# Optimization experiments

Hardware: AMD Instinct MI355X
Metric: run time of the kernel (lower is better)

Reference implementation:

```python
import jax, jax.numpy as jnp
import numpy as np

BATCH_SIZE = 512
N_PARTS = 4
TEMP_FAC = 0.1
D = 4096
EPS = 1e-6


def _static_indices():
    # bs and factor per the n_parts==4, batch_size!=12 branch
    bs = 4 * BATCH_SIZE
    factor = 10 * N_PARTS
    pos = np.arange(bs)
    active = pos[pos % (3 * N_PARTS) < N_PARTS]            # positions that contribute
    # i1..i6 = (pos + k*n_parts) % bs for k = 0..5
    I = (active[:, None] + np.arange(6)[None, :] * N_PARTS) % bs   # (P, 6)
    # denominator indices removed: (pos + k*n_parts) % bs for k = 0..factor*n_parts-1
    offs = (active[:, None] + np.arange(factor * N_PARTS)[None, :] * N_PARTS) % bs
    M = np.ones((active.shape[0], bs), dtype=np.float32)
    M[np.arange(active.shape[0])[:, None], offs] = 0.0     # (P, bs) denominator mask
    return I, M

_I, _M = _static_indices()
# symmetrical-loss pairs: (i1,i2),(i2,i3),(i1,i4),(i4,i5),(i5,i6),(i2,i5),(i3,i6)
_PAIRS = [(0, 1), (1, 2), (0, 3), (3, 4), (4, 5), (1, 4), (2, 5)]


def setup_inputs() -> dict:
    key = jax.random.key(0)
    reg_pred = jax.random.normal(key, (4 * BATCH_SIZE, D), dtype=jnp.float32)
    return {"reg_pred": reg_pred}


def reference(reg_pred):
    I = jnp.asarray(_I)
    M = jnp.asarray(_M)
    norms = jnp.linalg.norm(reg_pred, axis=1)              # (bs,)
    # torch CosineSimilarity: dot / max(||a||*||b||, eps)
    gram = reg_pred @ reg_pred.T                           # (bs, bs)
    S = gram / jnp.maximum(norms[:, None] * norms[None, :], EPS) / TEMP_FAC
    E = jnp.exp(S)                                         # (bs, bs)
    # denominator exp-sums for each anchor role k at each active position p
    Dsum = jnp.einsum('pkb,pb->pk', E[I], M)               # (P, 6)
    total = jnp.float32(0.0)
    for a, b in _PAIRS:
        num = S[I[:, a], I[:, b]]                          # (P,)
        en = jnp.exp(num)
        total = total + jnp.sum(-jnp.log(en / (en + Dsum[:, a]))
                                - jnp.log(en / (en + Dsum[:, b])))
    return total / (6 * BATCH_SIZE)
```

## Files before the change

### kernel.cpp

```cpp
#include <hip/hip_runtime.h>
#include <hip/hip_bf16.h>
#include <stdint.h>

#define NROWS 2048
#define DIM   4096
#define NACT  684
#define INV_TEMP 10.0f
#define NTILE 136
#define KSPLIT 4
#define KSEG  1024
#define KIT   16
#define FP8_SCALE 16.0f
#define PART_SCALE (1.0f / 256.0f)

#define WAITCNT_VM0   0x0F70
#define WAITCNT_VM4   0x0F74
#define WAITCNT_VM8   0x0F78

typedef __attribute__((ext_vector_type(4))) float floatx4;
typedef __attribute__((ext_vector_type(16))) float floatx16;
typedef __attribute__((ext_vector_type(4))) int intx4;
typedef __attribute__((ext_vector_type(8))) int intx8;
typedef __attribute__((ext_vector_type(8))) short shortx8;
typedef __attribute__((ext_vector_type(8))) unsigned short ushortx8;

static __device__ __forceinline__ unsigned short f32_to_bf16(float f) {
  union { float f; unsigned int u; } v; v.f = f;
  unsigned int u = v.u;
  unsigned int r = u + 0x7fffu + ((u >> 16) & 1u);
  return (unsigned short)(r >> 16);
}
static __device__ __forceinline__ float bf16_to_f32(unsigned short u) {
  union { unsigned int u; float f; } v; v.u = ((unsigned int)u) << 16;
  return v.f;
}
static __device__ __forceinline__ unsigned short f32_to_f16(float f) {
  _Float16 h = (_Float16)f;
  union { _Float16 h; unsigned short u; } v; v.h = h;
  return v.u;
}
static __device__ __forceinline__ float f16_to_f32(unsigned short u) {
  union { unsigned short u; _Float16 h; } v; v.u = u;
  return (float)v.h;
}

__global__ __launch_bounds__(256) void k_normconv_fp8(const float* __restrict__ X,
                                                      unsigned char* __restrict__ Yq,
                                                      float* __restrict__ T,
                                                      float* __restrict__ out) {
  const int row = blockIdx.x;
  if (threadIdx.x == 0) T[row] = 0.f;
  if (row == 0 && threadIdx.x == 64) *out = 0.f;
  const float4* xr = (const float4*)(X + (size_t)row * DIM);
  float4 v[4];
  float s = 0.f;
#pragma unroll
  for (int t = 0; t < 4; t++) {
    float4 w = xr[threadIdx.x + t * 256];
    v[t] = w;
    s += w.x * w.x + w.y * w.y + w.z * w.z + w.w * w.w;
  }
#pragma unroll
  for (int off = 32; off > 0; off >>= 1) s += __shfl_down(s, off, 64);
  __shared__ float wsum[4];
  if ((threadIdx.x & 63) == 0) wsum[threadIdx.x >> 6] = s;
  __syncthreads();
  const float total = wsum[0] + wsum[1] + wsum[2] + wsum[3];
  const float sc = FP8_SCALE / fmaxf(sqrtf(total), 1e-30f);
  unsigned int* yr = (unsigned int*)(Yq + (size_t)row * DIM);
#pragma unroll
  for (int t = 0; t < 4; t++) {
    float4 w = v[t];
    unsigned int r0 = __builtin_amdgcn_cvt_pk_fp8_f32(w.x * sc, w.y * sc, 0, false);
    r0 = __builtin_amdgcn_cvt_pk_fp8_f32(w.z * sc, w.w * sc, r0, true);
    yr[threadIdx.x + t * 256] = r0;
  }
}

__global__ __launch_bounds__(256) void k_gemm_mx(const unsigned char* __restrict__ Yq,
                                                 unsigned short* __restrict__ P) {
  __shared__ __attribute__((aligned(16))) unsigned char lds[3 * 16384];
  const int bid0 = blockIdx.x;
  const int bid = (bid0 & 7) * 68 + (bid0 >> 3);
  const int kz = bid & 3;
  const int t  = bid >> 2;
  int ti = 0, rem = t;
  while (rem >= 16 - ti) { rem -= 16 - ti; ti++; }
  const int tj = ti + rem;
  const int row0 = ti * 128;
  const int col0 = tj * 128;
  const int kbase = kz * KSEG;

  const int tid  = threadIdx.x;
  const int lane = tid & 63;
  const int wave = tid >> 6;
  const int wr = wave >> 1;
  const int wc = wave & 1;

  floatx16 zero = {0.f, 0.f, 0.f, 0.f, 0.f, 0.f, 0.f, 0.f,
                   0.f, 0.f, 0.f, 0.f, 0.f, 0.f, 0.f, 0.f};
  floatx16 acc[2][2];
#pragma unroll
  for (int i = 0; i < 2; i++)
#pragma unroll
    for (int j = 0; j < 2; j++) acc[i][j] = zero;

  const int r2  = tid >> 2;
  const int c16 = tid & 3;
  const unsigned int swst = (unsigned)(((r2 >> 1) & 3) << 4);
  const unsigned int colst = ((unsigned)(c16 << 4)) ^ swst;
  const unsigned char* gA = Yq + (size_t)(row0 + r2) * DIM + kbase + colst;
  const unsigned char* gB = Yq + (size_t)(col0 + r2) * DIM + kbase + colst;

#define ISSUE(st, koff)                                                                  \
  do {                                                                                   \
    __builtin_amdgcn_global_load_lds(                                                    \
        (const __attribute__((address_space(1))) void*)(gA + (koff)),                    \
        (__attribute__((address_space(3))) void*)(lds + (st) * 16384 + tid * 16),        \
        16, 0, 0);                                                                       \
    __builtin_amdgcn_global_load_lds(                                                    \
        (const __attribute__((address_space(1))) void*)(gA + (size_t)64 * DIM + (koff)), \
        (__attribute__((address_space(3))) void*)(lds + (st) * 16384 + 4096 + tid * 16), \
        16, 0, 0);                                                                       \
    __builtin_amdgcn_global_load_lds(                                                    \
        (const __attribute__((address_space(1))) void*)(gB + (koff)),                    \
        (__attribute__((address_space(3))) void*)(lds + (st) * 16384 + 8192 + tid * 16), \
        16, 0, 0);                                                                       \
    __builtin_amdgcn_global_load_lds(                                                    \
        (const __attribute__((address_space(1))) void*)(gB + (size_t)64 * DIM + (koff)), \
        (__attribute__((address_space(3))) void*)(lds + (st) * 16384 + 12288 + tid * 16),\
        16, 0, 0);                                                                       \
  } while (0)

#define COMPUTE(st)                                                                      \
  do {                                                                                   \
    const unsigned char* bA = lds + (st) * 16384;                                        \
    const unsigned char* bB = bA + 8192;                                                 \
    const unsigned int c0 = (unsigned)((lane >> 5) << 5);                                \
    intx8 af[2], bf[2];                                                                  \
    _Pragma("unroll")                                                                    \
    for (int mi = 0; mi < 2; mi++) {                                                     \
      const int r = wr * 64 + mi * 32 + (lane & 31);                                     \
      const unsigned int sw = (unsigned)(((r >> 1) & 3) << 4);                           \
      const unsigned char* base = bA + r * 64;                                           \
      intx4 lo = *(const intx4*)(base + (c0 ^ sw));                                      \
      intx4 hi = *(const intx4*)(base + ((c0 ^ sw) ^ 16u));                              \
      intx8 v;                                                                           \
      v[0] = lo[0]; v[1] = lo[1]; v[2] = lo[2]; v[3] = lo[3];                            \
      v[4] = hi[0]; v[5] = hi[1]; v[6] = hi[2]; v[7] = hi[3];                            \
      af[mi] = v;                                                                        \
    }                                                                                    \
    _Pragma("unroll")                                                                    \
    for (int ni = 0; ni < 2; ni++) {                                                     \
      const int r = wc * 64 + ni * 32 + (lane & 31);                                     \
      const unsigned int sw = (unsigned)(((r >> 1) & 3) << 4);                           \
      const unsigned char* base = bB + r * 64;                                           \
      intx4 lo = *(const intx4*)(base + (c0 ^ sw));                                      \
      intx4 hi = *(const intx4*)(base + ((c0 ^ sw) ^ 16u));                              \
      intx8 v;                                                                           \
      v[0] = lo[0]; v[1] = lo[1]; v[2] = lo[2]; v[3] = lo[3];                            \
      v[4] = hi[0]; v[5] = hi[1]; v[6] = hi[2]; v[7] = hi[3];                            \
      bf[ni] = v;                                                                        \
    }                                                                                    \
    _Pragma("unroll")                                                                    \
    for (int mi = 0; mi < 2; mi++)                                                       \
      _Pragma("unroll")                                                                  \
      for (int ni = 0; ni < 2; ni++)                                                     \
        acc[mi][ni] = __builtin_amdgcn_mfma_scale_f32_32x32x64_f8f6f4(                   \
            af[mi], bf[ni], acc[mi][ni], 0, 0, 0, 0x7F7F7F7F, 0, 0x7F7F7F7F);            \
  } while (0)

  ISSUE(0, 0);
  ISSUE(1, 64);
#pragma unroll
  for (int k = 0; k < KIT; k++) {
    const int cur = k % 3;
    if (k < KIT - 2) {
      ISSUE((k + 2) % 3, (k + 2) * 64);
      __builtin_amdgcn_s_waitcnt(WAITCNT_VM8);
    } else if (k == KIT - 2) {
      __builtin_amdgcn_s_waitcnt(WAITCNT_VM4);
    } else {
      __builtin_amdgcn_s_waitcnt(WAITCNT_VM0);
    }
    __builtin_amdgcn_sched_barrier(0);
    __builtin_amdgcn_s_barrier();
    COMPUTE(cur);
    if (k < KIT - 1) {
      __builtin_amdgcn_s_barrier();
      __builtin_amdgcn_sched_barrier(0);
    }
  }

#undef ISSUE
#undef COMPUTE

  unsigned short* dst = P + (size_t)(t * KSPLIT + kz) * 16384;
  const int cc = lane & 31;
  const int cr = (lane >> 5) * 4;
#pragma unroll
  for (int mi = 0; mi < 2; mi++) {
#pragma unroll
    for (int ni = 0; ni < 2; ni++) {
      const int col = wc * 64 + ni * 32 + cc;
#pragma unroll
      for (int q = 0; q < 4; q++) {
        const int row = wr * 64 + mi * 32 + q * 8 + cr;
        unsigned int d0 = (unsigned int)f32_to_bf16(acc[mi][ni][q * 4 + 0] * PART_SCALE) |
                          ((unsigned int)f32_to_bf16(acc[mi][ni][q * 4 + 1] * PART_SCALE) << 16);
        unsigned int d1 = (unsigned int)f32_to_bf16(acc[mi][ni][q * 4 + 2] * PART_SCALE) |
                          ((unsigned int)f32_to_bf16(acc[mi][ni][q * 4 + 3] * PART_SCALE) << 16);
        uint2 v; v.x = d0; v.y = d1;
        *(uint2*)(dst + (size_t)col * 128 + row) = v;
      }
    }
  }
}

__global__ __launch_bounds__(256) void k_combine(const unsigned short* __restrict__ P,
                                                 unsigned short* __restrict__ S,
                                                 float* __restrict__ T) {
  __shared__ float tileS[32][132];
  __shared__ float tileE[32][132];
  const int t = blockIdx.x;
  const int h = blockIdx.y;
  int ti = 0, rem = t;
  while (rem >= 16 - ti) { rem -= 16 - ti; ti++; }
  const int tj = ti + rem;
  const int gr = ti * 128, gc = tj * 128;
  const int c0 = h * 32;
  const int tid = threadIdx.x;
  const int cl = tid >> 3;
  const int q  = tid & 7;

  float acc[16];
#pragma unroll
  for (int j = 0; j < 16; j++) acc[j] = 0.f;
#pragma unroll
  for (int kz = 0; kz < KSPLIT; kz++) {
    const ushortx8* p = (const ushortx8*)(P + (size_t)(t * KSPLIT + kz) * 16384 +
                                          (size_t)(c0 + cl) * 128 + q * 16);
#pragma unroll
    for (int c = 0; c < 2; c++) {
      ushortx8 u = p[c];
#pragma unroll
      for (int e = 0; e < 8; e++) acc[c * 8 + e] += bf16_to_f32((unsigned short)u[e]);
    }
  }
  float cs = 0.f;
  unsigned short hv[16];
#pragma unroll
  for (int j = 0; j < 16; j++) {
    float v = acc[j] * INV_TEMP;
    float ev = __expf(v);
    hv[j] = f32_to_f16(v);
    tileS[cl][q * 16 + j] = v;
    tileE[cl][q * 16 + j] = ev;
    cs += ev;
  }
  {
    uint4* srow = (uint4*)(S + (size_t)(gc + c0 + cl) * NROWS + gr + q * 16);
#pragma unroll
    for (int u = 0; u < 2; u++) {
      uint4 w;
      w.x = (unsigned int)hv[u * 8 + 0] | ((unsigned int)hv[u * 8 + 1] << 16);
      w.y = (unsigned int)hv[u * 8 + 2] | ((unsigned int)hv[u * 8 + 3] << 16);
      w.z = (unsigned int)hv[u * 8 + 4] | ((unsigned int)hv[u * 8 + 5] << 16);
      w.w = (unsigned int)hv[u * 8 + 6] | ((unsigned int)hv[u * 8 + 7] << 16);
      srow[u] = w;
    }
  }
  cs += __shfl_xor(cs, 1, 64);
  cs += __shfl_xor(cs, 2, 64);
  cs += __shfl_xor(cs, 4, 64);
  if (q == 0) atomicAdd(&T[gc + c0 + cl], cs);

  if (ti != tj) {
    __syncthreads();
    const int r = tid >> 1;
    const int hh = tid & 1;
    float rs = 0.f;
    unsigned short hv2[16];
#pragma unroll
    for (int e = 0; e < 16; e++) {
      hv2[e] = f32_to_f16(tileS[hh * 16 + e][r]);
      rs += tileE[hh * 16 + e][r];
    }
    uint4* drow = (uint4*)(S + (size_t)(gr + r) * NROWS + gc + c0 + hh * 16);
#pragma unroll
    for (int u = 0; u < 2; u++) {
      uint4 w;
      w.x = (unsigned int)hv2[u * 8 + 0] | ((unsigned int)hv2[u * 8 + 1] << 16);
      w.y = (unsigned int)hv2[u * 8 + 2] | ((unsigned int)hv2[u * 8 + 3] << 16);
      w.z = (unsigned int)hv2[u * 8 + 4] | ((unsigned int)hv2[u * 8 + 5] << 16);
      w.w = (unsigned int)hv2[u * 8 + 6] | ((unsigned int)hv2[u * 8 + 7] << 16);
      drow[u] = w;
    }
    rs += __shfl_xor(rs, 1, 64);
    if (hh == 0) atomicAdd(&T[gr + r], rs);
  }
}

__global__ __launch_bounds__(384) void k_tail(const unsigned short* __restrict__ S,
                                              const float* __restrict__ T,
                                              float* __restrict__ out) {
  __shared__ float ds_s[6];
  const int p = blockIdx.x;
  const int a = 12 * (p >> 2) + (p & 3);
  const int tid = threadIdx.x;
  const int k = tid >> 6;
  const int lane = tid & 63;
  const int row = (a + 4 * k) & (NROWS - 1);
  const int m = a >> 2;
  const int c = a & 3;
  const uint2* sr = (const uint2*)(S + (size_t)row * NROWS);
  float s = 0.f;
  {
    uint2 v0 = sr[(m + lane) & 511];
    uint2 v1 = sr[(m + 64 + lane) & 511];
    unsigned short e0 = (c < 2) ? (unsigned short)(v0.x >> (16 * c))
                                : (unsigned short)(v0.y >> (16 * (c - 2)));
    unsigned short e1 = (c < 2) ? (unsigned short)(v1.x >> (16 * c))
                                : (unsigned short)(v1.y >> (16 * (c - 2)));
    s += __expf(f16_to_f32(e0)) + __expf(f16_to_f32(e1));
    if (lane < 32) {
      uint2 v2 = sr[(m + 128 + lane) & 511];
      unsigned short e2 = (c < 2) ? (unsigned short)(v2.x >> (16 * c))
                                  : (unsigned short)(v2.y >> (16 * (c - 2)));
      s += __expf(f16_to_f32(e2));
    }
  }
#pragma unroll
  for (int off = 32; off > 0; off >>= 1) s += __shfl_down(s, off, 64);
  if (lane == 0) ds_s[k] = T[row] - s;
  __syncthreads();

  float r = 0.f;
  if (tid < 7) {
    const int pa[7] = {0, 1, 0, 3, 4, 1, 2};
    const int pb[7] = {1, 2, 3, 4, 5, 4, 5};
    const int ra = (a + 4 * pa[tid]) & (NROWS - 1);
    const int rb = (a + 4 * pb[tid]) & (NROWS - 1);
    const float num = f16_to_f32(S[(size_t)ra * NROWS + rb]);
    const float en = __expf(num);
    r = __logf(en + ds_s[pa[tid]]) + __logf(en + ds_s[pb[tid]]) - 2.f * num;
  }
  if (tid < 64) {
    r += __shfl_down(r, 4, 64);
    r += __shfl_down(r, 2, 64);
    r += __shfl_down(r, 1, 64);
    if (tid == 0) atomicAdd(out, r * (1.0f / (6.0f * 512.0f)));
  }
}

__global__ __launch_bounds__(256) void k_normconv(const float* __restrict__ X,
                                                  unsigned short* __restrict__ Y) {
  const int row = blockIdx.x;
  const float4* xr = (const float4*)(X + (size_t)row * DIM);
  float4 v[4];
  float s = 0.f;
#pragma unroll
  for (int t = 0; t < 4; t++) {
    float4 w = xr[threadIdx.x + t * 256];
    v[t] = w;
    s += w.x * w.x + w.y * w.y + w.z * w.z + w.w * w.w;
  }
#pragma unroll
  for (int off = 32; off > 0; off >>= 1) s += __shfl_down(s, off, 64);
  __shared__ float wsum[4];
  if ((threadIdx.x & 63) == 0) wsum[threadIdx.x >> 6] = s;
  __syncthreads();
  const float total = wsum[0] + wsum[1] + wsum[2] + wsum[3];
  const float inv = 1.0f / fmaxf(sqrtf(total), 1e-30f);
  ushort4* yr = (ushort4*)(Y + (size_t)row * DIM);
#pragma unroll
  for (int t = 0; t < 4; t++) {
    float4 w = v[t];
    ushort4 o;
    o.x = f32_to_bf16(w.x * inv);
    o.y = f32_to_bf16(w.y * inv);
    o.z = f32_to_bf16(w.z * inv);
    o.w = f32_to_bf16(w.w * inv);
    yr[threadIdx.x + t * 256] = o;
  }
}

__global__ __launch_bounds__(256) void k_gemm(const unsigned short* __restrict__ Y,
                                              float* __restrict__ S) {
  __shared__ __attribute__((aligned(16))) unsigned short sA[128 * 32];
  __shared__ __attribute__((aligned(16))) unsigned short sB[128 * 32];
  const int tid  = threadIdx.x;
  const int lane = tid & 63;
  const int wave = tid >> 6;
  const int wr = wave >> 1;
  const int wc = wave & 1;
  const int row0 = blockIdx.y * 128;
  const int col0 = blockIdx.x * 128;

  floatx4 zero = {0.f, 0.f, 0.f, 0.f};
  floatx4 acc[4][4];
#pragma unroll
  for (int i = 0; i < 4; i++)
#pragma unroll
    for (int j = 0; j < 4; j++) acc[i][j] = zero;

  const int sr = tid >> 2;
  const int sc = (tid & 3) * 8;
  const unsigned short* gA0 = Y + (size_t)(row0 + sr) * DIM + sc;
  const unsigned short* gA1 = gA0 + (size_t)64 * DIM;
  const unsigned short* gB0 = Y + (size_t)(col0 + sr) * DIM + sc;
  const unsigned short* gB1 = gB0 + (size_t)64 * DIM;

  const int fr = lane & 15;
  const int fc = (lane >> 4) * 8;

  for (int k0 = 0; k0 < DIM; k0 += 32) {
    __builtin_amdgcn_global_load_lds(
        (const __attribute__((address_space(1))) void*)(gA0 + k0),
        (__attribute__((address_space(3))) void*)(sA + tid * 8), 16, 0, 0);
    __builtin_amdgcn_global_load_lds(
        (const __attribute__((address_space(1))) void*)(gA1 + k0),
        (__attribute__((address_space(3))) void*)(sA + 2048 + tid * 8), 16, 0, 0);
    __builtin_amdgcn_global_load_lds(
        (const __attribute__((address_space(1))) void*)(gB0 + k0),
        (__attribute__((address_space(3))) void*)(sB + tid * 8), 16, 0, 0);
    __builtin_amdgcn_global_load_lds(
        (const __attribute__((address_space(1))) void*)(gB1 + k0),
        (__attribute__((address_space(3))) void*)(sB + 2048 + tid * 8), 16, 0, 0);
    __syncthreads();

    shortx8 af[4], bf[4];
#pragma unroll
    for (int mi = 0; mi < 4; mi++)
      af[mi] = *(const shortx8*)(sA + (wr * 64 + mi * 16 + fr) * 32 + fc);
#pragma unroll
    for (int ni = 0; ni < 4; ni++)
      bf[ni] = *(const shortx8*)(sB + (wc * 64 + ni * 16 + fr) * 32 + fc);
#pragma unroll
    for (int mi = 0; mi < 4; mi++)
#pragma unroll
      for (int ni = 0; ni < 4; ni++)
        acc[mi][ni] = __builtin_amdgcn_mfma_f32_16x16x32_bf16(af[mi], bf[ni], acc[mi][ni], 0, 0, 0);
    __syncthreads();
  }

  const int cc  = lane & 15;
  const int cr4 = (lane >> 4) * 4;
#pragma unroll
  for (int mi = 0; mi < 4; mi++) {
    const int row = row0 + wr * 64 + mi * 16 + cr4;
#pragma unroll
    for (int ni = 0; ni < 4; ni++) {
      const int col = col0 + wc * 64 + ni * 16 + cc;
      float* dst = S + (size_t)row * NROWS + col;
#pragma unroll
      for (int r = 0; r < 4; r++) dst[(size_t)r * NROWS] = acc[mi][ni][r] * INV_TEMP;
    }
  }
}

__global__ __launch_bounds__(256) void k_rowsum(const float* __restrict__ S,
                                                float* __restrict__ T) {
  const int row = blockIdx.x;
  const float* sr = S + (size_t)row * NROWS;
  float s = 0.f;
  for (int b = threadIdx.x; b < NROWS; b += 256) s += __expf(sr[b]);
#pragma unroll
  for (int off = 32; off > 0; off >>= 1) s += __shfl_down(s, off, 64);
  __shared__ float wsum[4];
  if ((threadIdx.x & 63) == 0) wsum[threadIdx.x >> 6] = s;
  __syncthreads();
  if (threadIdx.x == 0) T[row] = wsum[0] + wsum[1] + wsum[2] + wsum[3];
}

__global__ __launch_bounds__(64) void k_dsum(const float* __restrict__ S,
                                             const float* __restrict__ T,
                                             float* __restrict__ Ds) {
  const int p = blockIdx.x;
  const int k = blockIdx.y;
  const int a = 12 * (p >> 2) + (p & 3);
  const int lane = threadIdx.x;
  const int row = (a + 4 * k) & (NROWS - 1);
  const int m = a >> 2;
  const int c = a & 3;
  const float4* sr4 = (const float4*)(S + (size_t)row * NROWS);
  float s = 0.f;
  {
    float4 v0 = sr4[(m + lane) & 511];
    float4 v1 = sr4[(m + 64 + lane) & 511];
    float e0 = c == 0 ? v0.x : c == 1 ? v0.y : c == 2 ? v0.z : v0.w;
    float e1 = c == 0 ? v1.x : c == 1 ? v1.y : c == 2 ? v1.z : v1.w;
    s += __expf(e0) + __expf(e1);
    if (lane < 32) {
      float4 v2 = sr4[(m + 128 + lane) & 511];
      float e2 = c == 0 ? v2.x : c == 1 ? v2.y : c == 2 ? v2.z : v2.w;
      s += __expf(e2);
    }
  }
#pragma unroll
  for (int off = 32; off > 0; off >>= 1) s += __shfl_down(s, off, 64);
  if (lane == 0) Ds[p * 6 + k] = T[row] - s;
}

__global__ __launch_bounds__(256) void k_final(const float* __restrict__ S,
                                               const float* __restrict__ Ds,
                                               float* __restrict__ out) {
  const int pa[7] = {0, 1, 0, 3, 4, 1, 2};
  const int pb[7] = {1, 2, 3, 4, 5, 4, 5};
  const int idx = blockIdx.x * 256 + threadIdx.x;
  float s = 0.f;
  if (idx < NACT * 7) {
    const int p = idx / 7;
    const int q = idx - p * 7;
    const int a0 = 12 * (p >> 2) + (p & 3);
    const int ra = (a0 + 4 * pa[q]) & (NROWS - 1);
    const int rb = (a0 + 4 * pb[q]) & (NROWS - 1);
    const float num = S[(size_t)ra * NROWS + rb];
    const float en = __expf(num);
    s = __logf(en + Ds[p * 6 + pa[q]]) + __logf(en + Ds[p * 6 + pb[q]]) - 2.f * num;
  }
#pragma unroll
  for (int off = 32; off > 0; off >>= 1) s += __shfl_down(s, off, 64);
  if ((threadIdx.x & 63) == 0) atomicAdd(out, s * (1.0f / (6.0f * 512.0f)));
}

extern "C" void kernel_launch(void* const* d_in, const int* in_sizes, int n_in,
                              void* d_out, int out_size, void* d_ws, size_t ws_size,
                              hipStream_t stream) {
  const float* X = (const float*)d_in[0];
  char* ws = (char*)d_ws;
  float* out = (float*)d_out;

  const size_t pOff = (size_t)32 * 1024 * 1024;
  const size_t pBytes = (size_t)NTILE * KSPLIT * 16384 * 2;
  const size_t needA = pOff + pBytes + 8192 + NACT * 6 * 4 + 256;

  if (ws_size >= needA) {
    unsigned char* Yq = (unsigned char*)ws;
    unsigned short* S16 = (unsigned short*)(ws + (size_t)16 * 1024 * 1024);
    unsigned short* P = (unsigned short*)(ws + pOff);
    float* T  = (float*)(ws + pOff + pBytes);
    hipLaunchKernelGGL(k_normconv_fp8, dim3(NROWS), dim3(256), 0, stream, X, Yq, T, out);
    hipLaunchKernelGGL(k_gemm_mx, dim3(NTILE * KSPLIT), dim3(256), 0, stream, Yq, P);
    hipLaunchKernelGGL(k_combine, dim3(NTILE, 4), dim3(256), 0, stream, P, S16, T);
    hipLaunchKernelGGL(k_tail, dim3(NACT), dim3(384), 0, stream, S16, T, out);
  } else {
    unsigned short* Y = (unsigned short*)ws;
    float* S = (float*)(ws + (size_t)16 * 1024 * 1024);
    float* T  = (float*)(ws + pOff);
    float* Ds = (float*)(ws + pOff + 8192);
    hipMemsetAsync(out, 0, sizeof(float), stream);
    hipLaunchKernelGGL(k_normconv, dim3(NROWS), dim3(256), 0, stream, X, Y);
    hipLaunchKernelGGL(k_gemm, dim3(16, 16), dim3(256), 0, stream, Y, S);
    hipLaunchKernelGGL(k_rowsum, dim3(NROWS), dim3(256), 0, stream, S, T);
    hipLaunchKernelGGL(k_dsum, dim3(NACT, 6), dim3(64), 0, stream, S, T, Ds);
    hipLaunchKernelGGL(k_final, dim3((NACT * 7 + 255) / 256), dim3(256), 0, stream, S, Ds, out);
  }
}
```

Measured before the change: 112.4 us.

## Replace split-K GEMM plus combine with full-K 64x64 tile GEMM and fused epilogue

Drops the split-K FP8 MFMA GEMM, which wrote bf16 partial tiles, and the separate combine kernel. A single kernel now computes full-K 64x64 upper-triangular tiles across 528 blocks using a 4-stage global_load_lds pipeline. It applies the temperature scaling and exp in the epilogue, writes f16 S and its transpose through LDS, and atomically accumulates row and column exp sums. This removes the partial-tile memory round trip and one launch, at the cost of smaller tiles with less data reuse, one MFMA per wave per step, and a longer K loop per block.

```diff
diff --git a/kernel.cpp b/kernel.cpp
--- a/kernel.cpp
+++ b/kernel.cpp
@@ -6,16 +6,16 @@
 #define DIM   4096
 #define NACT  684
 #define INV_TEMP 10.0f
-#define NTILE 136
-#define KSPLIT 4
-#define KSEG  1024
-#define KIT   16
+#define NPANEL 32
+#define NTILE64 528
+#define NK 64
 #define FP8_SCALE 16.0f
-#define PART_SCALE (1.0f / 256.0f)
+#define OUT_SCALE (INV_TEMP / 256.0f)
 
 #define WAITCNT_VM0   0x0F70
+#define WAITCNT_VM2   0x0F72
 #define WAITCNT_VM4   0x0F74
-#define WAITCNT_VM8   0x0F78
+#define WAITCNT_VM6   0x0F76
 
 typedef __attribute__((ext_vector_type(4))) float floatx4;
 typedef __attribute__((ext_vector_type(16))) float floatx16;
@@ -77,19 +77,17 @@
   }
 }
 
-__global__ __launch_bounds__(256) void k_gemm_mx(const unsigned char* __restrict__ Yq,
-                                                 unsigned short* __restrict__ P) {
-  __shared__ __attribute__((aligned(16))) unsigned char lds[3 * 16384];
+__global__ __launch_bounds__(256) void k_gemm_full(const unsigned char* __restrict__ Yq,
+                                                   unsigned short* __restrict__ S,
+                                                   float* __restrict__ T) {
+  __shared__ __attribute__((aligned(16))) unsigned char lds[32768];
   const int bid0 = blockIdx.x;
-  const int bid = (bid0 & 7) * 68 + (bid0 >> 3);
-  const int kz = bid & 3;
-  const int t  = bid >> 2;
+  const int t = (bid0 & 7) * 66 + (bid0 >> 3);
   int ti = 0, rem = t;
-  while (rem >= 16 - ti) { rem -= 16 - ti; ti++; }
+  while (rem >= NPANEL - ti) { rem -= NPANEL - ti; ti++; }
   const int tj = ti + rem;
-  const int row0 = ti * 128;
-  const int col0 = tj * 128;
-  const int kbase = kz * KSEG;
+  const int gr = ti * 64;
+  const int gc = tj * 64;
 
   const int tid  = threadIdx.x;
   const int lane = tid & 63;
@@ -97,96 +95,72 @@
   const int wr = wave >> 1;
   const int wc = wave & 1;
 
-  floatx16 zero = {0.f, 0.f, 0.f, 0.f, 0.f, 0.f, 0.f, 0.f,
-                   0.f, 0.f, 0.f, 0.f, 0.f, 0.f, 0.f, 0.f};
-  floatx16 acc[2][2];
-#pragma unroll
-  for (int i = 0; i < 2; i++)
-#pragma unroll
-    for (int j = 0; j < 2; j++) acc[i][j] = zero;
+  floatx16 acc = {0.f, 0.f, 0.f, 0.f, 0.f, 0.f, 0.f, 0.f,
+                  0.f, 0.f, 0.f, 0.f, 0.f, 0.f, 0.f, 0.f};
 
   const int r2  = tid >> 2;
   const int c16 = tid & 3;
   const unsigned int swst = (unsigned)(((r2 >> 1) & 3) << 4);
   const unsigned int colst = ((unsigned)(c16 << 4)) ^ swst;
-  const unsigned char* gA = Yq + (size_t)(row0 + r2) * DIM + kbase + colst;
-  const unsigned char* gB = Yq + (size_t)(col0 + r2) * DIM + kbase + colst;
+  const unsigned char* gA = Yq + (size_t)(gr + r2) * DIM + colst;
+  const unsigned char* gB = Yq + (size_t)(gc + r2) * DIM + colst;
 
 #define ISSUE(st, koff)                                                                  \
   do {                                                                                   \
     __builtin_amdgcn_global_load_lds(                                                    \
         (const __attribute__((address_space(1))) void*)(gA + (koff)),                    \
-        (__attribute__((address_space(3))) void*)(lds + (st) * 16384 + tid * 16),        \
-        16, 0, 0);                                                                       \
-    __builtin_amdgcn_global_load_lds(                                                    \
-        (const __attribute__((address_space(1))) void*)(gA + (size_t)64 * DIM + (koff)), \
-        (__attribute__((address_space(3))) void*)(lds + (st) * 16384 + 4096 + tid * 16), \
+        (__attribute__((address_space(3))) void*)(lds + (st) * 8192 + tid * 16),         \
         16, 0, 0);                                                                       \
     __builtin_amdgcn_global_load_lds(                                                    \
         (const __attribute__((address_space(1))) void*)(gB + (koff)),                    \
-        (__attribute__((address_space(3))) void*)(lds + (st) * 16384 + 8192 + tid * 16), \
-        16, 0, 0);                                                                       \
-    __builtin_amdgcn_global_load_lds(                                                    \
-        (const __attribute__((address_space(1))) void*)(gB + (size_t)64 * DIM + (koff)), \
-        (__attribute__((address_space(3))) void*)(lds + (st) * 16384 + 12288 + tid * 16),\
+        (__attribute__((address_space(3))) void*)(lds + (st) * 8192 + 4096 + tid * 16),  \
         16, 0, 0);                                                                       \
   } while (0)
 
 #define COMPUTE(st)                                                                      \
   do {                                                                                   \
-    const unsigned char* bA = lds + (st) * 16384;                                        \
-    const unsigned char* bB = bA + 8192;                                                 \
+    const unsigned char* bA = lds + (st) * 8192;                                         \
+    const unsigned char* bB = bA + 4096;                                                 \
     const unsigned int c0 = (unsigned)((lane >> 5) << 5);                                \
-    intx8 af[2], bf[2];                                                                  \
-    _Pragma("unroll")                                                                    \
-    for (int mi = 0; mi < 2; mi++) {                                                     \
-      const int r = wr * 64 + mi * 32 + (lane & 31);                                     \
-      const unsigned int sw = (unsigned)(((r >> 1) & 3) << 4);                           \
-      const unsigned char* base = bA + r * 64;                                           \
-      intx4 lo = *(const intx4*)(base + (c0 ^ sw));                                      \
-      intx4 hi = *(const intx4*)(base + ((c0 ^ sw) ^ 16u));                              \
-      intx8 v;                                                                           \
-      v[0] = lo[0]; v[1] = lo[1]; v[2] = lo[2]; v[3] = lo[3];                            \
-      v[4] = hi[0]; v[5] = hi[1]; v[6] = hi[2]; v[7] = hi[3];                            \
-      af[mi] = v;                                                                        \
-    }                                                                                    \
-    _Pragma("unroll")                                                                    \
-    for (int ni = 0; ni < 2; ni++) {                                                     \
-      const int r = wc * 64 + ni * 32 + (lane & 31);                                     \
-      const unsigned int sw = (unsigned)(((r >> 1) & 3) << 4);                           \
-      const unsigned char* base = bB + r * 64;                                           \
-      intx4 lo = *(const intx4*)(base + (c0 ^ sw));                                      \
-      intx4 hi = *(const intx4*)(base + ((c0 ^ sw) ^ 16u));                              \
-      intx8 v;                                                                           \
-      v[0] = lo[0]; v[1] = lo[1]; v[2] = lo[2]; v[3] = lo[3];                            \
-      v[4] = hi[0]; v[5] = hi[1]; v[6] = hi[2]; v[7] = hi[3];                            \
-      bf[ni] = v;                                                                        \
-    }                                                                                    \
-    _Pragma("unroll")                                                                    \
-    for (int mi = 0; mi < 2; mi++)                                                       \
-      _Pragma("unroll")                                                                  \
-      for (int ni = 0; ni < 2; ni++)                                                     \
-        acc[mi][ni] = __builtin_amdgcn_mfma_scale_f32_32x32x64_f8f6f4(                   \
-            af[mi], bf[ni], acc[mi][ni], 0, 0, 0, 0x7F7F7F7F, 0, 0x7F7F7F7F);            \
+    const int rA = wr * 32 + (lane & 31);                                                \
+    const int rB = wc * 32 + (lane & 31);                                                \
+    const unsigned int swA = (unsigned)(((rA >> 1) & 3) << 4);                           \
+    const unsigned int swB = (unsigned)(((rB >> 1) & 3) << 4);                           \
+    const unsigned char* baseA = bA + rA * 64;                                           \
+    const unsigned char* baseB = bB + rB * 64;                                           \
+    intx4 alo = *(const intx4*)(baseA + (c0 ^ swA));                                     \
+    intx4 ahi = *(const intx4*)(baseA + ((c0 ^ swA) ^ 16u));                             \
+    intx4 blo = *(const intx4*)(baseB + (c0 ^ swB));                                     \
+    intx4 bhi = *(const intx4*)(baseB + ((c0 ^ swB) ^ 16u));                             \
+    intx8 af, bf;                                                                        \
+    af[0] = alo[0]; af[1] = alo[1]; af[2] = alo[2]; af[3] = alo[3];                      \
+    af[4] = ahi[0]; af[5] = ahi[1]; af[6] = ahi[2]; af[7] = ahi[3];                      \
+    bf[0] = blo[0]; bf[1] = blo[1]; bf[2] = blo[2]; bf[3] = blo[3];                      \
+    bf[4] = bhi[0]; bf[5] = bhi[1]; bf[6] = bhi[2]; bf[7] = bhi[3];                      \
+    acc = __builtin_amdgcn_mfma_scale_f32_32x32x64_f8f6f4(                               \
+        af, bf, acc, 0, 0, 0, 0x7F7F7F7F, 0, 0x7F7F7F7F);                                \
   } while (0)
 
   ISSUE(0, 0);
   ISSUE(1, 64);
-#pragma unroll
-  for (int k = 0; k < KIT; k++) {
-    const int cur = k % 3;
-    if (k < KIT - 2) {
-      ISSUE((k + 2) % 3, (k + 2) * 64);
-      __builtin_amdgcn_s_waitcnt(WAITCNT_VM8);
-    } else if (k == KIT - 2) {
+  ISSUE(2, 128);
+#pragma unroll 4
+  for (int k = 0; k < NK; k++) {
+    const int cur = k & 3;
+    if (k < NK - 3) {
+      ISSUE((k + 3) & 3, (k + 3) * 64);
+      __builtin_amdgcn_s_waitcnt(WAITCNT_VM6);
+    } else if (k == NK - 3) {
       __builtin_amdgcn_s_waitcnt(WAITCNT_VM4);
+    } else if (k == NK - 2) {
+      __builtin_amdgcn_s_waitcnt(WAITCNT_VM2);
     } else {
       __builtin_amdgcn_s_waitcnt(WAITCNT_VM0);
     }
     __builtin_amdgcn_sched_barrier(0);
     __builtin_amdgcn_s_barrier();
     COMPUTE(cur);
-    if (k < KIT - 1) {
+    if (k < NK - 1) {
       __builtin_amdgcn_s_barrier();
       __builtin_amdgcn_sched_barrier(0);
     }
@@ -195,109 +169,64 @@
 #undef ISSUE
 #undef COMPUTE
 
-  unsigned short* dst = P + (size_t)(t * KSPLIT + kz) * 16384;
-  const int cc = lane & 31;
-  const int cr = (lane >> 5) * 4;
-#pragma unroll
-  for (int mi = 0; mi < 2; mi++) {
-#pragma unroll
-    for (int ni = 0; ni < 2; ni++) {
-      const int col = wc * 64 + ni * 32 + cc;
-#pragma unroll
-      for (int q = 0; q < 4; q++) {
-        const int row = wr * 64 + mi * 32 + q * 8 + cr;
-        unsigned int d0 = (unsigned int)f32_to_bf16(acc[mi][ni][q * 4 + 0] * PART_SCALE) |
-                          ((unsigned int)f32_to_bf16(acc[mi][ni][q * 4 + 1] * PART_SCALE) << 16);
-        unsigned int d1 = (unsigned int)f32_to_bf16(acc[mi][ni][q * 4 + 2] * PART_SCALE) |
-                          ((unsigned int)f32_to_bf16(acc[mi][ni][q * 4 + 3] * PART_SCALE) << 16);
-        uint2 v; v.x = d0; v.y = d1;
-        *(uint2*)(dst + (size_t)col * 128 + row) = v;
-      }
-    }
-  }
-}
-
-__global__ __launch_bounds__(256) void k_combine(const unsigned short* __restrict__ P,
-                                                 unsigned short* __restrict__ S,
-                                                 float* __restrict__ T) {
-  __shared__ float tileS[32][132];
-  __shared__ float tileE[32][132];
-  const int t = blockIdx.x;
-  const int h = blockIdx.y;
-  int ti = 0, rem = t;
-  while (rem >= 16 - ti) { rem -= 16 - ti; ti++; }
-  const int tj = ti + rem;
-  const int gr = ti * 128, gc = tj * 128;
-  const int c0 = h * 32;
-  const int tid = threadIdx.x;
-  const int cl = tid >> 3;
-  const int q  = tid & 7;
-
-  float acc[16];
-#pragma unroll
-  for (int j = 0; j < 16; j++) acc[j] = 0.f;
-#pragma unroll
-  for (int kz = 0; kz < KSPLIT; kz++) {
-    const ushortx8* p = (const ushortx8*)(P + (size_t)(t * KSPLIT + kz) * 16384 +
-                                          (size_t)(c0 + cl) * 128 + q * 16);
-#pragma unroll
-    for (int c = 0; c < 2; c++) {
-      ushortx8 u = p[c];
-#pragma unroll
-      for (int e = 0; e < 8; e++) acc[c * 8 + e] += bf16_to_f32((unsigned short)u[e]);
-    }
-  }
-  float cs = 0.f;
-  unsigned short hv[16];
-#pragma unroll
-  for (int j = 0; j < 16; j++) {
-    float v = acc[j] * INV_TEMP;
-    float ev = __expf(v);
-    hv[j] = f32_to_f16(v);
-    tileS[cl][q * 16 + j] = v;
-    tileE[cl][q * 16 + j] = ev;
-    cs += ev;
-  }
+  unsigned short* tile16 = (unsigned short*)lds;
+  float* tileE   = (float*)(lds + 8448);
+  float* colpart = (float*)(lds + 25088);
+  __syncthreads();
+
   {
-    uint4* srow = (uint4*)(S + (size_t)(gc + c0 + cl) * NROWS + gr + q * 16);
-#pragma unroll
-    for (int u = 0; u < 2; u++) {
-      uint4 w;
-      w.x = (unsigned int)hv[u * 8 + 0] | ((unsigned int)hv[u * 8 + 1] << 16);
-      w.y = (unsigned int)hv[u * 8 + 2] | ((unsigned int)hv[u * 8 + 3] << 16);
-      w.z = (unsigned int)hv[u * 8 + 4] | ((unsigned int)hv[u * 8 + 5] << 16);
-      w.w = (unsigned int)hv[u * 8 + 6] | ((unsigned int)hv[u * 8 + 7] << 16);
-      srow[u] = w;
-    }
-  }
-  cs += __shfl_xor(cs, 1, 64);
-  cs += __shfl_xor(cs, 2, 64);
-  cs += __shfl_xor(cs, 4, 64);
-  if (q == 0) atomicAdd(&T[gc + c0 + cl], cs);
+    const int col = wc * 32 + (lane & 31);
+    float evsum = 0.f;
+#pragma unroll
+    for (int i = 0; i < 16; i++) {
+      const int row = wr * 32 + (i & 3) + 8 * (i >> 2) + 4 * (lane >> 5);
+      const float v = acc[i] * OUT_SCALE;
+      const float ev = __expf(v);
+      tile16[row * 66 + col] = f32_to_f16(v);
+      tileE[row * 65 + col] = ev;
+      evsum += ev;
+    }
+    evsum += __shfl_xor(evsum, 32, 64);
+    if (lane < 32) colpart[wr * 64 + col] = evsum;
+  }
+  __syncthreads();
+
+  if (tid < 64) atomicAdd(&T[gc + tid], colpart[tid] + colpart[64 + tid]);
+
+  {
+    const int r = tid >> 2, seg = tid & 3;
+    const unsigned int* q = (const unsigned int*)tile16 + (r * 33 + seg * 8);
+    uint4 w0, w1;
+    w0.x = q[0]; w0.y = q[1]; w0.z = q[2]; w0.w = q[3];
+    w1.x = q[4]; w1.y = q[5]; w1.z = q[6]; w1.w = q[7];
+    uint4* dst = (uint4*)(S + (size_t)(gr + r) * NROWS + gc + seg * 16);
+    dst[0] = w0; dst[1] = w1;
+  }
 
   if (ti != tj) {
-    __syncthreads();
-    const int r = tid >> 1;
-    const int hh = tid & 1;
-    float rs = 0.f;
-    unsigned short hv2[16];
-#pragma unroll
-    for (int e = 0; e < 16; e++) {
-      hv2[e] = f32_to_f16(tileS[hh * 16 + e][r]);
-      rs += tileE[hh * 16 + e][r];
-    }
-    uint4* drow = (uint4*)(S + (size_t)(gr + r) * NROWS + gc + c0 + hh * 16);
-#pragma unroll
-    for (int u = 0; u < 2; u++) {
-      uint4 w;
-      w.x = (unsigned int)hv2[u * 8 + 0] | ((unsigned int)hv2[u * 8 + 1] << 16);
-      w.y = (unsigned int)hv2[u * 8 + 2] | ((unsigned int)hv2[u * 8 + 3] << 16);
-      w.z = (unsigned int)hv2[u * 8 + 4] | ((unsigned int)hv2[u * 8 + 5] << 16);
-      w.w = (unsigned int)hv2[u * 8 + 6] | ((unsigned int)hv2[u * 8 + 7] << 16);
-      drow[u] = w;
-    }
-    rs += __shfl_xor(rs, 1, 64);
-    if (hh == 0) atomicAdd(&T[gr + r], rs);
+    if (tid < 64) {
+      float rs = 0.f;
+#pragma unroll 8
+      for (int c = 0; c < 64; c++) rs += tileE[tid * 65 + c];
+      atomicAdd(&T[gr + tid], rs);
+    }
+    {
+      const int c = tid >> 2, seg = tid & 3;
+      unsigned short tmp[16];
+#pragma unroll
+      for (int k = 0; k < 16; k++) tmp[k] = tile16[(seg * 16 + k) * 66 + c];
+      uint4 w0, w1;
+      w0.x = (unsigned int)tmp[0]  | ((unsigned int)tmp[1]  << 16);
+      w0.y = (unsigned int)tmp[2]  | ((unsigned int)tmp[3]  << 16);
+      w0.z = (unsigned int)tmp[4]  | ((unsigned int)tmp[5]  << 16);
+      w0.w = (unsigned int)tmp[6]  | ((unsigned int)tmp[7]  << 16);
+      w1.x = (unsigned int)tmp[8]  | ((unsigned int)tmp[9]  << 16);
+      w1.y = (unsigned int)tmp[10] | ((unsigned int)tmp[11] << 16);
+      w1.z = (unsigned int)tmp[12] | ((unsigned int)tmp[13] << 16);
+      w1.w = (unsigned int)tmp[14] | ((unsigned int)tmp[15] << 16);
+      uint4* dst = (uint4*)(S + (size_t)(gc + c) * NROWS + gr + seg * 16);
+      dst[0] = w0; dst[1] = w1;
+    }
   }
 }
 
@@ -532,17 +461,14 @@
   float* out = (float*)d_out;
 
   const size_t pOff = (size_t)32 * 1024 * 1024;
-  const size_t pBytes = (size_t)NTILE * KSPLIT * 16384 * 2;
-  const size_t needA = pOff + pBytes + 8192 + NACT * 6 * 4 + 256;
+  const size_t needA = pOff + 8192 + 256;
 
   if (ws_size >= needA) {
     unsigned char* Yq = (unsigned char*)ws;
     unsigned short* S16 = (unsigned short*)(ws + (size_t)16 * 1024 * 1024);
-    unsigned short* P = (unsigned short*)(ws + pOff);
-    float* T  = (float*)(ws + pOff + pBytes);
+    float* T  = (float*)(ws + pOff);
     hipLaunchKernelGGL(k_normconv_fp8, dim3(NROWS), dim3(256), 0, stream, X, Yq, T, out);
-    hipLaunchKernelGGL(k_gemm_mx, dim3(NTILE * KSPLIT), dim3(256), 0, stream, Yq, P);
-    hipLaunchKernelGGL(k_combine, dim3(NTILE, 4), dim3(256), 0, stream, P, S16, T);
+    hipLaunchKernelGGL(k_gemm_full, dim3(NTILE64), dim3(256), 0, stream, Yq, S16, T);
     hipLaunchKernelGGL(k_tail, dim3(NACT), dim3(384), 0, stream, S16, T, out);
   } else {
     unsigned short* Y = (unsigned short*)ws;
```

Result: faster. 108.7 us (-3.3%).
